# Performance work log

Hardware: AMD Instinct MI355X
Metric: run time of the kernel (lower is better)

The kernel has to match this reference:

```python
import jax, jax.numpy as jnp
import numpy as np

WS = 4        # window_size
SHIFT = 2     # shift
NHEADS = 8


def setup_inputs():
    key = jax.random.key(0)
    k = jax.random.split(key, 5)
    N, C, H, W = 16, 512, 96, 96
    x = jax.random.normal(k[0], (N, C, H, W), dtype=jnp.float32)
    # nn.MultiheadAttention parameters
    in_proj_w = jax.random.normal(k[1], (3 * C, C), dtype=jnp.float32) * 0.02
    in_proj_b = jax.random.normal(k[2], (3 * C,), dtype=jnp.float32) * 0.02
    out_w = jax.random.normal(k[3], (C, C), dtype=jnp.float32) * 0.02
    out_b = jax.random.normal(k[4], (C,), dtype=jnp.float32) * 0.02
    return {"x": x, "in_proj_w": in_proj_w, "in_proj_b": in_proj_b,
            "out_w": out_w, "out_b": out_b}


def _split_window(x, ws):
    # replicates torch: cat(split(x, ws, dim=3), dim=2); cat(split(x, ws, dim=2), dim=0)
    N, C, Hp, Wp = x.shape
    nh, nw = Hp // ws, Wp // ws
    x = x.reshape(N, C, nh, ws, nw, ws)      # n c ib wi jb wj
    x = x.transpose(4, 2, 0, 1, 3, 5)        # jb ib n c wi wj (col-block outermost in batch)
    return x.reshape(nw * nh * N, C, ws, ws), nh, nw


def _concat_window(x, nh, nw, ws):
    # inverse of _split_window, replicating torch chunk/cat order
    N = x.shape[0] // (nh * nw)
    C = x.shape[1]
    x = x.reshape(nw, nh, N, C, ws, ws)      # jb ib n c wi wj
    x = x.transpose(2, 3, 1, 4, 0, 5)        # n c ib wi jb wj
    return x.reshape(N, C, nh * ws, nw * ws)


def _mha(xt, mask_f, in_proj_w, in_proj_b, out_w, out_b):
    # xt: (B, L, C); mask_f: (B, L) FLOAT key_padding_mask -> added to logits (torch semantics)
    B, L, C = xt.shape
    d = C // NHEADS
    qkv = xt @ in_proj_w.T + in_proj_b                     # (B, L, 3C)
    q, k, v = jnp.split(qkv, 3, axis=-1)
    heads = lambda t: t.reshape(B, L, NHEADS, d).transpose(0, 2, 1, 3)  # (B, H, L, d)
    q, k, v = heads(q), heads(k), heads(v)
    scale = float(1.0 / np.sqrt(d))
    scores = jnp.einsum('bhqd,bhkd->bhqk', q, k) * scale
    scores = scores + mask_f[:, None, None, :]             # additive float key mask
    attn = jax.nn.softmax(scores, axis=-1)
    o = jnp.einsum('bhqk,bhkd->bhqd', attn, v)
    o = o.transpose(0, 2, 1, 3).reshape(B, L, C)
    return o @ out_w.T + out_b


def reference(x, in_proj_w, in_proj_b, out_w, out_b):
    N, C, H, W = x.shape
    ws = WS
    pad_h, pad_w = ws - H % ws, ws - W % ws   # note: pads a full window even when divisible
    x = jnp.pad(x, ((0, 0), (0, 0), (0, pad_h), (0, pad_w)))
    x = jnp.roll(x, (SHIFT, SHIFT), axis=(2, 3))
    # BUG-FAITHFUL: source overwrites the boolean mask with a second roll of x,
    # so the "mask" is the doubly-rolled float feature map.
    mask = jnp.roll(x, (SHIFT, SHIFT), axis=(2, 3))
    xw, nh, nw = _split_window(x, ws)
    mw, _, _ = _split_window(mask, ws)
    B = xw.shape[0]
    xt = xw.reshape(B, C, ws * ws).transpose(0, 2, 1)      # (B, L=ws*ws, C)
    mask_f = mw[:, 0].reshape(B, ws * ws)                  # channel-0 float "mask"
    ot = _mha(xt, mask_f, in_proj_w, in_proj_b, out_w, out_b)
    ow = ot.transpose(0, 2, 1).reshape(B, C, ws, ws)
    out = _concat_window(ow, nh, nw, ws)
    out = jnp.roll(out, (-SHIFT, -SHIFT), axis=(2, 3))
    return out[:, :, :H, :W]
```

## Files before the change

kernel.cpp:

```cpp
#include <hip/hip_runtime.h>
#include <cstdint>


typedef __attribute__((ext_vector_type(8))) __bf16 bf16x8;
typedef __attribute__((ext_vector_type(8))) uint16_t u16x8;
typedef __attribute__((ext_vector_type(4))) float f32x4;

__device__ __forceinline__ uint16_t f2bf(float f) {
  union { float f; uint32_t u; } c; c.f = f;
  uint32_t r = c.u + 0x7FFFu + ((c.u >> 16) & 1u);
  return (uint16_t)(r >> 16);
}
__device__ __forceinline__ float bf2f(uint16_t u) {
  union { uint32_t u; float f; } c; c.u = ((uint32_t)u) << 16;
  return c.f;
}

__device__ __forceinline__ void g2lds16(const void* g, void* lds) {
  __builtin_amdgcn_global_load_lds(
      (const __attribute__((address_space(1))) uint32_t*)(uintptr_t)g,
      (__attribute__((address_space(3))) uint32_t*)(uintptr_t)lds,
      16, 0, 0);
}

__global__ void cvt_weights(const float* __restrict__ w1, const float* __restrict__ w2,
                            uint16_t* __restrict__ o1, uint16_t* __restrict__ o2) {
  int i = blockIdx.x * 256 + threadIdx.x;
  if (i < 786432) o1[i] = f2bf(w1[i]);
  if (i < 262144) o2[i] = f2bf(w2[i]);
}

__global__ __launch_bounds__(256) void gather_kernel(
    const float* __restrict__ x, uint16_t* __restrict__ xbf, int n0) {
  __shared__ float tile[64][65];
  const int z = blockIdx.z;
  const int g = z / 100, hh = z % 100;
  const int c0 = blockIdx.y * 64, ww0 = blockIdx.x * 64;
  const int n = n0 + g;
  const int hp = (hh >= 2) ? hh - 2 : hh + 98;
  const bool hok = hp < 96;
  const int t = threadIdx.x;
  const int lane = t & 63, grp = t >> 6;

  const int ww = ww0 + lane;
  const int wp = (ww >= 2) ? ww - 2 : ww + 98;
  const bool wok = hok && (ww < 100) && (wp < 96);
  const float* xb = x + ((size_t)n * 512) * 9216 + (size_t)hp * 96 + wp;
#pragma unroll
  for (int i = 0; i < 16; ++i) {
    int c = grp + i * 4;
    tile[c][lane] = wok ? xb[(size_t)(c0 + c) * 9216] : 0.f;
  }
  __syncthreads();
#pragma unroll
  for (int i = 0; i < 16; ++i) {
    int wl = grp + i * 4;
    int www = ww0 + wl;
    if (www < 100) {
      int m = g * 10000 + hh * 100 + www;
      xbf[(size_t)m * 512 + c0 + lane] = f2bf(tile[lane][wl]);
    }
  }
}

template <int EPI>
__global__ __launch_bounds__(256, 2) void gemm_bf16(
    const uint16_t* __restrict__ A, const uint16_t* __restrict__ B,
    const float* __restrict__ bias, uint16_t* __restrict__ Cbf,
    float* __restrict__ Cout, int K, int Ntot, int rowLimit, int colLimit, int n0) {
  __shared__ alignas(16) uint16_t At[128 * 64];
  __shared__ alignas(16) uint16_t Bt[128 * 64];
  const int t = threadIdx.x;
  const int lane = t & 63, wv = t >> 6;
  const int wr = wv >> 1, wc = wv & 1;
  const int lr = lane & 15, lg = lane >> 4;
  const int bm = blockIdx.y, bn = blockIdx.x;

  f32x4 acc[4][4];
#pragma unroll
  for (int mi = 0; mi < 4; ++mi)
#pragma unroll
    for (int ni = 0; ni < 4; ++ni) acc[mi][ni] = (f32x4){0.f, 0.f, 0.f, 0.f};

  for (int k0 = 0; k0 < K; k0 += 64) {
#pragma unroll
    for (int i = 0; i < 4; ++i) {
      int e = i * 256 + t;
      int row = e >> 3, c8 = (e & 7) << 3;
      const uint16_t* ga = A + (size_t)(bm * 128 + row) * K + k0 + c8;
      const uint16_t* gb = B + (size_t)(bn * 128 + row) * K + k0 + c8;
      int ldsoff = (i * 256 + (wv << 6)) << 3;
      g2lds16(ga, &At[ldsoff]);
      g2lds16(gb, &Bt[ldsoff]);
    }
    __syncthreads();
#pragma unroll
    for (int kk = 0; kk < 64; kk += 32) {
      bf16x8 av[4], bv[4];
#pragma unroll
      for (int mi = 0; mi < 4; ++mi)
        av[mi] = *(const bf16x8*)&At[(wr * 64 + mi * 16 + lr) * 64 + kk + lg * 8];
#pragma unroll
      for (int ni = 0; ni < 4; ++ni)
        bv[ni] = *(const bf16x8*)&Bt[(wc * 64 + ni * 16 + lr) * 64 + kk + lg * 8];
#pragma unroll
      for (int mi = 0; mi < 4; ++mi)
#pragma unroll
        for (int ni = 0; ni < 4; ++ni)
          acc[mi][ni] = __builtin_amdgcn_mfma_f32_16x16x32_bf16(
              av[mi], bv[ni], acc[mi][ni], 0, 0, 0);
    }
    __syncthreads();
  }

  if (EPI == 0) {
#pragma unroll
    for (int mi = 0; mi < 4; ++mi) {
      int row = bm * 128 + wr * 64 + mi * 16 + lg * 4;
#pragma unroll
      for (int ni = 0; ni < 4; ++ni) {
        int col = bn * 128 + wc * 64 + ni * 16 + lr;
        float bb = bias[col];
#pragma unroll
        for (int r = 0; r < 4; ++r)
          if (row + r < rowLimit)
            Cbf[(size_t)(row + r) * Ntot + col] = f2bf(acc[mi][ni][r] + bb);
      }
    }
  } else {
#pragma unroll
    for (int ni = 0; ni < 4; ++ni) {
      int tok = bn * 128 + wc * 64 + ni * 16 + lr;
      if (tok < colLimit) {
        int g = tok / 10000, rem = tok % 10000;
        int hh = rem / 100, ww = rem % 100;
        if (hh >= 2 && hh < 98 && ww >= 2 && ww < 98) {
          size_t base = ((size_t)(n0 + g) * 512) * 9216 + (size_t)(hh - 2) * 96 + (ww - 2);
#pragma unroll
          for (int mi = 0; mi < 4; ++mi) {
            int c = bm * 128 + wr * 64 + mi * 16 + lg * 4;
#pragma unroll
            for (int r = 0; r < 4; ++r)
              Cout[base + (size_t)(c + r) * 9216] = acc[mi][ni][r] + bias[c + r];
          }
        }
      }
    }
  }
}

__global__ __launch_bounds__(128) void attn_kernel(
    const uint16_t* __restrict__ qkv, const float* __restrict__ x,
    uint16_t* __restrict__ obuf, int n0) {
  __shared__ alignas(16) uint16_t sq[16][1536];
  __shared__ float smask[16];
  const int b = blockIdx.x;
  const int g = b / 625, wid = b % 625;
  const int ib = wid / 25, jb = wid % 25;
  const int t = threadIdx.x;
  const int mbase = g * 10000 + ib * 400 + jb * 4;

#pragma unroll
  for (int it = 0; it < 24; ++it) {
    int e = it * 128 + t;
    int l = e / 192;
    int off = (e - l * 192) * 8;
    int m = mbase + (l >> 2) * 100 + (l & 3);
    *(uint4*)&sq[l][off] = *(const uint4*)&qkv[(size_t)m * 1536 + off];
  }
  if (t < 16) {
    int hh = ib * 4 + (t >> 2), ww = jb * 4 + (t & 3);
    int a = (hh >= 4) ? hh - 4 : hh + 96;
    int c = (ww >= 4) ? ww - 4 : ww + 96;
    smask[t] = (a < 96 && c < 96)
                   ? x[((size_t)(n0 + g) * 512) * 9216 + (size_t)a * 96 + c]
                   : 0.f;
  }
  __syncthreads();

  const int h = t >> 4, qi = t & 15;
  float q[64];
#pragma unroll
  for (int d8 = 0; d8 < 8; ++d8) {
    u16x8 v = *(const u16x8*)&sq[qi][h * 64 + d8 * 8];
#pragma unroll
    for (int j = 0; j < 8; ++j) q[d8 * 8 + j] = bf2f(v[j]);
  }
  float s[16];
  float mx = -1e30f;
#pragma unroll
  for (int ki = 0; ki < 16; ++ki) {
    float a = 0.f;
#pragma unroll
    for (int d8 = 0; d8 < 8; ++d8) {
      u16x8 kv = *(const u16x8*)&sq[ki][512 + h * 64 + d8 * 8];
#pragma unroll
      for (int j = 0; j < 8; ++j) a += q[d8 * 8 + j] * bf2f(kv[j]);
    }
    s[ki] = a * 0.125f + smask[ki];
    mx = fmaxf(mx, s[ki]);
  }
  float sum = 0.f;
#pragma unroll
  for (int ki = 0; ki < 16; ++ki) { s[ki] = __expf(s[ki] - mx); sum += s[ki]; }
  const float inv = 1.f / sum;
  float o[64];
#pragma unroll
  for (int d = 0; d < 64; ++d) o[d] = 0.f;
#pragma unroll
  for (int ki = 0; ki < 16; ++ki) {
    float w = s[ki] * inv;
#pragma unroll
    for (int d8 = 0; d8 < 8; ++d8) {
      u16x8 vv = *(const u16x8*)&sq[ki][1024 + h * 64 + d8 * 8];
#pragma unroll
      for (int j = 0; j < 8; ++j) o[d8 * 8 + j] += w * bf2f(vv[j]);
    }
  }
  const int m = mbase + (qi >> 2) * 100 + (qi & 3);
#pragma unroll
  for (int d8 = 0; d8 < 8; ++d8) {
    alignas(16) uint16_t tmp[8];
#pragma unroll
    for (int j = 0; j < 8; ++j) tmp[j] = f2bf(o[d8 * 8 + j]);
    *(uint4*)&obuf[(size_t)m * 512 + h * 64 + d8 * 8] = *(uint4*)tmp;
  }
}

extern "C" void kernel_launch(void* const* d_in, const int* in_sizes, int n_in,
                              void* d_out, int out_size, void* d_ws, size_t ws_size,
                              hipStream_t stream) {
  const float* x    = (const float*)d_in[0];
  const float* wq   = (const float*)d_in[1];
  const float* bq   = (const float*)d_in[2];
  const float* wo   = (const float*)d_in[3];
  const float* bo   = (const float*)d_in[4];
  float* out = (float*)d_out;
  uint8_t* ws = (uint8_t*)d_ws;

  uint16_t* wq_bf = (uint16_t*)ws;
  uint16_t* wo_bf = (uint16_t*)(ws + 1572864);
  uint8_t* bufbase = ws + 2097152;

  int G = 16;
  while (G > 1) {
    int Mg = G * 10000;
    int Mp = ((Mg + 127) / 128) * 128;
    size_t need = (size_t)2097152 + (size_t)Mp * 4096;
    if (need <= ws_size) break;
    G >>= 1;
  }
  const int Mg = G * 10000;
  const int Mp = ((Mg + 127) / 128) * 128;
  uint16_t* xo   = (uint16_t*)bufbase;
  uint16_t* qkvb = (uint16_t*)(bufbase + (size_t)Mp * 1024);

  cvt_weights<<<dim3(3072), dim3(256), 0, stream>>>(wq, wo, wq_bf, wo_bf);

  for (int n0 = 0; n0 < 16; n0 += G) {
    gather_kernel<<<dim3(2, 8, G * 100), dim3(256), 0, stream>>>(x, xo, n0);
    gemm_bf16<0><<<dim3(12, Mp / 128), dim3(256), 0, stream>>>(
        xo, wq_bf, bq, qkvb, nullptr, 512, 1536, Mg, 0, 0);
    attn_kernel<<<dim3(G * 625), dim3(128), 0, stream>>>(qkvb, x, xo, n0);
    gemm_bf16<1><<<dim3(Mp / 128, 4), dim3(256), 0, stream>>>(
        wo_bf, xo, bo, nullptr, out, 512, 0, 512, Mg, n0);
  }
  (void)in_sizes; (void)n_in; (void)out_size;
}
```

Before: 1.056 ms.

## Replace bf16 GEMM with 256x256-tile double-buffered ping-pong MFMA kernel

Replaces the 128x128 single-buffered GEMM with a 512-thread kernel that computes 256x256 output tiles. It double-buffers K-slices in a 128KB LDS region with an XOR swizzle and interleaves global-to-LDS staging with four MFMA quadrants per step, using explicit barriers, waitcnt and setprio. It also remaps block IDs so that neighbouring tiles are grouped per XCD. The aim is to raise MFMA utilisation and operand reuse and to hide load latency; the cost is much higher LDS use (one block per CU) and padding of M to 256.

```diff
diff --git a/kernel.cpp b/kernel.cpp
--- a/kernel.cpp
+++ b/kernel.cpp
@@ -22,6 +22,9 @@
       (__attribute__((address_space(3))) uint32_t*)(uintptr_t)lds,
       16, 0, 0);
 }
+
+#define CFENCE asm volatile("" ::: "memory")
+#define BAR do { CFENCE; __builtin_amdgcn_s_barrier(); CFENCE; } while (0)
 
 __global__ void cvt_weights(const float* __restrict__ w1, const float* __restrict__ w2,
                             uint16_t* __restrict__ o1, uint16_t* __restrict__ o2) {
@@ -63,85 +66,142 @@
   }
 }
 
-template <int EPI>
-__global__ __launch_bounds__(256, 2) void gemm_bf16(
+template <int EPI, int NB, int MODE>
+__global__ __launch_bounds__(512, 2) void gemm8(
     const uint16_t* __restrict__ A, const uint16_t* __restrict__ B,
     const float* __restrict__ bias, uint16_t* __restrict__ Cbf,
-    float* __restrict__ Cout, int K, int Ntot, int rowLimit, int colLimit, int n0) {
-  __shared__ alignas(16) uint16_t At[128 * 64];
-  __shared__ alignas(16) uint16_t Bt[128 * 64];
+    float* __restrict__ Cout, int Mg, int n0) {
+  __shared__ alignas(16) uint16_t lds[65536];
   const int t = threadIdx.x;
-  const int lane = t & 63, wv = t >> 6;
-  const int wr = wv >> 1, wc = wv & 1;
+  const int w = t >> 6, lane = t & 63;
+  const int wr = w >> 2, wc = w & 3;
   const int lr = lane & 15, lg = lane >> 4;
-  const int bm = blockIdx.y, bn = blockIdx.x;
-
-  f32x4 acc[4][4];
-#pragma unroll
-  for (int mi = 0; mi < 4; ++mi)
+
+  const int nwg = gridDim.x, bid = blockIdx.x;
+  const int q = nwg >> 3, r = nwg & 7;
+  const int xc = bid & 7, li = bid >> 3;
+  const int wg = (xc < r ? xc * (q + 1) : r * (q + 1) + (xc - r) * q) + li;
+  int bm, bn;
+  if (MODE == 0) { bm = wg / NB; bn = wg % NB; }
+  else           { bm = wg % NB; bn = wg / NB; }
+
+  auto STAGE = [&](int kt, int h) {
+    const uint16_t* src = (h < 2) ? A : B;
+    const int row0 = ((h < 2) ? bm * 256 : bn * 256) + (h & 1) * 128;
+    const int base = ((h < 2) ? 0 : 32768) + (kt & 1) * 16384 + (h & 1) * 8192;
+#pragma unroll
+    for (int i = 0; i < 2; ++i) {
+      int e = i * 512 + t;
+      int row = e >> 3, slot = e & 7;
+      const uint16_t* g = src + (size_t)(row0 + row) * 512 + kt * 64 +
+                          ((slot ^ (row & 7)) << 3);
+      g2lds16(g, &lds[base + ((i * 512 + w * 64) << 3)]);
+    }
+  };
+  auto LDA = [&](int cur, int mi, int k2) -> bf16x8 {
+    int row = wr * 128 + mi * 16 + lr;
+    int byte = cur * 32768 + row * 128 + (((k2 * 32 + lg * 8) * 2) ^ ((row & 7) << 4));
+    return *(const bf16x8*)((const char*)lds + byte);
+  };
+  auto LDB = [&](int cur, int ni, int k2) -> bf16x8 {
+    int row = wc * 64 + ni * 16 + lr;
+    int byte = 65536 + cur * 32768 + row * 128 +
+               (((k2 * 32 + lg * 8) * 2) ^ ((row & 7) << 4));
+    return *(const bf16x8*)((const char*)lds + byte);
+  };
+
+  f32x4 acc[8][4];
+#pragma unroll
+  for (int mi = 0; mi < 8; ++mi)
 #pragma unroll
     for (int ni = 0; ni < 4; ++ni) acc[mi][ni] = (f32x4){0.f, 0.f, 0.f, 0.f};
 
-  for (int k0 = 0; k0 < K; k0 += 64) {
-#pragma unroll
-    for (int i = 0; i < 4; ++i) {
-      int e = i * 256 + t;
-      int row = e >> 3, c8 = (e & 7) << 3;
-      const uint16_t* ga = A + (size_t)(bm * 128 + row) * K + k0 + c8;
-      const uint16_t* gb = B + (size_t)(bn * 128 + row) * K + k0 + c8;
-      int ldsoff = (i * 256 + (wv << 6)) << 3;
-      g2lds16(ga, &At[ldsoff]);
-      g2lds16(gb, &Bt[ldsoff]);
-    }
-    __syncthreads();
-#pragma unroll
-    for (int kk = 0; kk < 64; kk += 32) {
-      bf16x8 av[4], bv[4];
-#pragma unroll
-      for (int mi = 0; mi < 4; ++mi)
-        av[mi] = *(const bf16x8*)&At[(wr * 64 + mi * 16 + lr) * 64 + kk + lg * 8];
-#pragma unroll
-      for (int ni = 0; ni < 4; ++ni)
-        bv[ni] = *(const bf16x8*)&Bt[(wc * 64 + ni * 16 + lr) * 64 + kk + lg * 8];
-#pragma unroll
-      for (int mi = 0; mi < 4; ++mi)
-#pragma unroll
-        for (int ni = 0; ni < 4; ++ni)
-          acc[mi][ni] = __builtin_amdgcn_mfma_f32_16x16x32_bf16(
-              av[mi], bv[ni], acc[mi][ni], 0, 0, 0);
-    }
-    __syncthreads();
-  }
+  STAGE(0, 0); STAGE(0, 1); STAGE(0, 2); STAGE(0, 3);
+  STAGE(1, 0); STAGE(1, 1);
+  asm volatile("s_waitcnt vmcnt(4)" ::: "memory");
+  BAR;
+
+#define MFMAQ(AF, BF, MIOFF, NIOFF)                                        \
+  __builtin_amdgcn_s_setprio(1);                                           \
+  _Pragma("unroll") for (int mi = 0; mi < 4; ++mi)                         \
+  _Pragma("unroll") for (int ni = 0; ni < 2; ++ni)                         \
+  _Pragma("unroll") for (int k2 = 0; k2 < 2; ++k2)                         \
+      acc[mi + MIOFF][ni + NIOFF] = __builtin_amdgcn_mfma_f32_16x16x32_bf16( \
+          AF[mi][k2], BF[ni][k2], acc[mi + MIOFF][ni + NIOFF], 0, 0, 0);   \
+  __builtin_amdgcn_s_setprio(0);
+
+  for (int j = 0; j < 8; ++j) {
+    const int cur = j & 1;
+    bf16x8 a0[4][2], a1[4][2], b0[2][2], b1[2][2];
+#pragma unroll
+    for (int mi = 0; mi < 4; ++mi)
+#pragma unroll
+      for (int k2 = 0; k2 < 2; ++k2) a0[mi][k2] = LDA(cur, mi, k2);
+#pragma unroll
+    for (int ni = 0; ni < 2; ++ni)
+#pragma unroll
+      for (int k2 = 0; k2 < 2; ++k2) b0[ni][k2] = LDB(cur, ni, k2);
+    if (j + 1 < 8) STAGE(j + 1, 2);
+    BAR;
+    __builtin_amdgcn_sched_barrier(0);
+    MFMAQ(a0, b0, 0, 0);
+    BAR;
+#pragma unroll
+    for (int mi = 0; mi < 4; ++mi)
+#pragma unroll
+      for (int k2 = 0; k2 < 2; ++k2) a1[mi][k2] = LDA(cur, mi + 4, k2);
+#pragma unroll
+    for (int ni = 0; ni < 2; ++ni)
+#pragma unroll
+      for (int k2 = 0; k2 < 2; ++k2) b1[ni][k2] = LDB(cur, ni + 2, k2);
+    if (j + 1 < 8) STAGE(j + 1, 3);
+    BAR;
+    __builtin_amdgcn_sched_barrier(0);
+    MFMAQ(a1, b1, 4, 2);
+    BAR;
+    if (j + 2 < 8) STAGE(j + 2, 0);
+    BAR;
+    __builtin_amdgcn_sched_barrier(0);
+    MFMAQ(a0, b1, 0, 2);
+    BAR;
+    if (j + 2 < 8) STAGE(j + 2, 1);
+    if (j < 6) { asm volatile("s_waitcnt vmcnt(4)" ::: "memory"); }
+    else       { asm volatile("s_waitcnt vmcnt(0)" ::: "memory"); }
+    BAR;
+    __builtin_amdgcn_sched_barrier(0);
+    MFMAQ(a1, b0, 4, 0);
+    BAR;
+  }
+#undef MFMAQ
 
   if (EPI == 0) {
 #pragma unroll
-    for (int mi = 0; mi < 4; ++mi) {
-      int row = bm * 128 + wr * 64 + mi * 16 + lg * 4;
-#pragma unroll
-      for (int ni = 0; ni < 4; ++ni) {
-        int col = bn * 128 + wc * 64 + ni * 16 + lr;
-        float bb = bias[col];
-#pragma unroll
-        for (int r = 0; r < 4; ++r)
-          if (row + r < rowLimit)
-            Cbf[(size_t)(row + r) * Ntot + col] = f2bf(acc[mi][ni][r] + bb);
+    for (int ni = 0; ni < 4; ++ni) {
+      int col = bn * 256 + wc * 64 + ni * 16 + lr;
+      float bb = bias[col];
+#pragma unroll
+      for (int mi = 0; mi < 8; ++mi) {
+        int row = bm * 256 + wr * 128 + mi * 16 + lg * 4;
+#pragma unroll
+        for (int rr = 0; rr < 4; ++rr)
+          Cbf[(size_t)(row + rr) * 1536 + col] = f2bf(acc[mi][ni][rr] + bb);
       }
     }
   } else {
 #pragma unroll
     for (int ni = 0; ni < 4; ++ni) {
-      int tok = bn * 128 + wc * 64 + ni * 16 + lr;
-      if (tok < colLimit) {
+      int tok = bn * 256 + wc * 64 + ni * 16 + lr;
+      if (tok < Mg) {
         int g = tok / 10000, rem = tok % 10000;
         int hh = rem / 100, ww = rem % 100;
         if (hh >= 2 && hh < 98 && ww >= 2 && ww < 98) {
           size_t base = ((size_t)(n0 + g) * 512) * 9216 + (size_t)(hh - 2) * 96 + (ww - 2);
 #pragma unroll
-          for (int mi = 0; mi < 4; ++mi) {
-            int c = bm * 128 + wr * 64 + mi * 16 + lg * 4;
-#pragma unroll
-            for (int r = 0; r < 4; ++r)
-              Cout[base + (size_t)(c + r) * 9216] = acc[mi][ni][r] + bias[c + r];
+          for (int mi = 0; mi < 8; ++mi) {
+            int c = bm * 256 + wr * 128 + mi * 16 + lg * 4;
+#pragma unroll
+            for (int rr = 0; rr < 4; ++rr)
+              Cout[base + (size_t)(c + rr) * 9216] = acc[mi][ni][rr] + bias[c + rr];
           }
         }
       }
@@ -179,12 +239,12 @@
   __syncthreads();
 
   const int h = t >> 4, qi = t & 15;
-  float q[64];
+  float qv[64];
 #pragma unroll
   for (int d8 = 0; d8 < 8; ++d8) {
     u16x8 v = *(const u16x8*)&sq[qi][h * 64 + d8 * 8];
 #pragma unroll
-    for (int j = 0; j < 8; ++j) q[d8 * 8 + j] = bf2f(v[j]);
+    for (int j = 0; j < 8; ++j) qv[d8 * 8 + j] = bf2f(v[j]);
   }
   float s[16];
   float mx = -1e30f;
@@ -195,7 +255,7 @@
     for (int d8 = 0; d8 < 8; ++d8) {
       u16x8 kv = *(const u16x8*)&sq[ki][512 + h * 64 + d8 * 8];
 #pragma unroll
-      for (int j = 0; j < 8; ++j) a += q[d8 * 8 + j] * bf2f(kv[j]);
+      for (int j = 0; j < 8; ++j) a += qv[d8 * 8 + j] * bf2f(kv[j]);
     }
     s[ki] = a * 0.125f + smask[ki];
     mx = fmaxf(mx, s[ki]);
@@ -209,12 +269,12 @@
   for (int d = 0; d < 64; ++d) o[d] = 0.f;
 #pragma unroll
   for (int ki = 0; ki < 16; ++ki) {
-    float w = s[ki] * inv;
+    float wgt = s[ki] * inv;
 #pragma unroll
     for (int d8 = 0; d8 < 8; ++d8) {
       u16x8 vv = *(const u16x8*)&sq[ki][1024 + h * 64 + d8 * 8];
 #pragma unroll
-      for (int j = 0; j < 8; ++j) o[d8 * 8 + j] += w * bf2f(vv[j]);
+      for (int j = 0; j < 8; ++j) o[d8 * 8 + j] += wgt * bf2f(vv[j]);
     }
   }
   const int m = mbase + (qi >> 2) * 100 + (qi & 3);
@@ -230,11 +290,11 @@
 extern "C" void kernel_launch(void* const* d_in, const int* in_sizes, int n_in,
                               void* d_out, int out_size, void* d_ws, size_t ws_size,
                               hipStream_t stream) {
-  const float* x    = (const float*)d_in[0];
-  const float* wq   = (const float*)d_in[1];
-  const float* bq   = (const float*)d_in[2];
-  const float* wo   = (const float*)d_in[3];
-  const float* bo   = (const float*)d_in[4];
+  const float* x  = (const float*)d_in[0];
+  const float* wq = (const float*)d_in[1];
+  const float* bq = (const float*)d_in[2];
+  const float* wo = (const float*)d_in[3];
+  const float* bo = (const float*)d_in[4];
   float* out = (float*)d_out;
   uint8_t* ws = (uint8_t*)d_ws;
 
@@ -245,13 +305,13 @@
   int G = 16;
   while (G > 1) {
     int Mg = G * 10000;
-    int Mp = ((Mg + 127) / 128) * 128;
+    int Mp = ((Mg + 255) / 256) * 256;
     size_t need = (size_t)2097152 + (size_t)Mp * 4096;
     if (need <= ws_size) break;
     G >>= 1;
   }
   const int Mg = G * 10000;
-  const int Mp = ((Mg + 127) / 128) * 128;
+  const int Mp = ((Mg + 255) / 256) * 256;
   uint16_t* xo   = (uint16_t*)bufbase;
   uint16_t* qkvb = (uint16_t*)(bufbase + (size_t)Mp * 1024);
 
@@ -259,11 +319,11 @@
 
   for (int n0 = 0; n0 < 16; n0 += G) {
     gather_kernel<<<dim3(2, 8, G * 100), dim3(256), 0, stream>>>(x, xo, n0);
-    gemm_bf16<0><<<dim3(12, Mp / 128), dim3(256), 0, stream>>>(
-        xo, wq_bf, bq, qkvb, nullptr, 512, 1536, Mg, 0, 0);
+    gemm8<0, 6, 0><<<dim3((Mp / 256) * 6), dim3(512), 0, stream>>>(
+        xo, wq_bf, bq, qkvb, nullptr, Mg, n0);
     attn_kernel<<<dim3(G * 625), dim3(128), 0, stream>>>(qkvb, x, xo, n0);
-    gemm_bf16<1><<<dim3(Mp / 128, 4), dim3(256), 0, stream>>>(
-        wo_bf, xo, bo, nullptr, out, 512, 0, 512, Mg, n0);
+    gemm8<1, 2, 1><<<dim3((Mp / 256) * 2), dim3(512), 0, stream>>>(
+        wo_bf, xo, bo, nullptr, out, Mg, n0);
   }
   (void)in_sizes; (void)n_in; (void)out_size;
 }
```

Measured after the change: 1.063 ms. Within noise of the previous version (+0.6%).
